# Kernel optimization log

Hardware: AMD Instinct MI355X
Metric: run time of the kernel (lower is better)

The kernel has to match this reference:

```python
import jax, jax.numpy as jnp
import numpy as np

B, N, DIM = 4, 2048, 512
H, DH = 8, 64  # n_heads, dim_head; inner = H*DH = 512
SCALE = DH ** -0.5


def setup_inputs() -> dict:
    key = jax.random.key(0)
    k1, k2, k3 = jax.random.split(key, 3)
    inner = H * DH
    X = jax.random.normal(k1, (B, N, DIM), dtype=jnp.float32)
    W_qkv = jax.random.normal(k2, (DIM, 3 * inner), dtype=jnp.float32) * (DIM ** -0.5)
    W_out = jax.random.normal(k3, (inner, DIM), dtype=jnp.float32) * (inner ** -0.5)
    b_out = jnp.zeros((DIM,), dtype=jnp.float32)
    return {"X": X, "W_qkv": W_qkv, "W_out": W_out, "b_out": b_out}


def reference(X, W_qkv, W_out, b_out):
    # X: (b, n, dim)
    qkv = X @ W_qkv                      # (b, n, 3*h*d)
    q, k, v = jnp.split(qkv, 3, axis=-1)
    def to_heads(t):
        b, n, _ = t.shape
        return t.reshape(b, n, H, DH).transpose(0, 2, 1, 3)  # (b, h, n, d)
    q, k, v = to_heads(q), to_heads(k), to_heads(v)
    # NOTE: original computes scores[n, m] = k_n . q_m and softmaxes over m (query axis)
    scores = jnp.einsum('bhnd,bhmd->bhnm', k, q) * SCALE     # (b, h, n_k, m_q)
    att = jax.nn.softmax(scores, axis=-1)
    # out token axis is the KEY index n: out[n, d] = sum_e att[n, e] * v[e, d]
    out = jnp.einsum('bhne,bhed->bhnd', att, v)              # (b, h, n, d)
    out = out.transpose(0, 2, 1, 3).reshape(X.shape[0], X.shape[1], H * DH)  # (b, n, h*d)
    return out @ W_out + b_out
```

## Files before the change

kernel.cpp:

```cpp
#include <hip/hip_runtime.h>
#include <hip/hip_bf16.h>

typedef __bf16 bf16_t;
typedef bf16_t bf16x8 __attribute__((ext_vector_type(8)));
typedef bf16_t bf16x4v __attribute__((ext_vector_type(4)));
typedef float f32x4 __attribute__((ext_vector_type(4)));
typedef float f32x16 __attribute__((ext_vector_type(16)));
typedef int i32x4 __attribute__((ext_vector_type(4)));

#define B_SZ 4
#define N_TOK 2048
#define DIM 512
#define H_N 8
#define DH 64
#define INNER 512
#define M_ROWS 8192
#define NQKV 1536
#define K_FOLD 0.18033688011112042f

#define GLD_LDS16(gp, lp)                                          \
  __builtin_amdgcn_global_load_lds(                                \
      (const __attribute__((address_space(1))) void*)(gp),         \
      (__attribute__((address_space(3))) void*)(lp), 16, 0, 0)

__device__ __forceinline__ float fexp2(float x) {
#if __has_builtin(__builtin_amdgcn_exp2f)
  return __builtin_amdgcn_exp2f(x);
#else
  float r;
  asm volatile("v_exp_f32 %0, %1\n\ts_nop 1" : "=v"(r) : "v"(x));
  return r;
#endif
}

__device__ __forceinline__ int cvtpk_bf16(float lo, float hi) {
  int r;
  asm("v_cvt_pk_bf16_f32 %0, %1, %2" : "=v"(r) : "v"(lo), "v"(hi));
  return r;
}

__device__ __forceinline__ void permswap32(int& a, int& b) {
  asm volatile("v_permlane32_swap_b32 %0, %1" : "+v"(a), "+v"(b));
}


__global__ void f32_to_bf16_kernel(const float* __restrict__ src,
                                   bf16_t* __restrict__ dst, int n4) {
  int i = blockIdx.x * blockDim.x + threadIdx.x;
  int stride = gridDim.x * blockDim.x;
  for (; i < n4; i += stride) {
    float4 f = reinterpret_cast<const float4*>(src)[i];
    bf16x4v o;
    o.x = (bf16_t)f.x; o.y = (bf16_t)f.y; o.z = (bf16_t)f.z; o.w = (bf16_t)f.w;
    reinterpret_cast<bf16x4v*>(dst)[i] = o;
  }
}

__global__ void transpose_f32_to_bf16_kernel(const float* __restrict__ src,
                                             bf16_t* __restrict__ dst, int R, int C) {
  int t = blockIdx.x * blockDim.x + threadIdx.x;
  if (t >= R * C) return;
  int r = t / C, c = t - r * C;
  dst[(size_t)c * R + r] = (bf16_t)src[t];
}

template <int MODE>
__global__ __launch_bounds__(256) void gemm_bf16_kernel(
    const bf16_t* __restrict__ A, const bf16_t* __restrict__ Bt,
    int M, int Nn, int K,
    bf16_t* __restrict__ qb, bf16_t* __restrict__ kb, bf16_t* __restrict__ vtb,
    float* __restrict__ outF, const float* __restrict__ bias) {
  __shared__ bf16_t As[128 * 64];
  __shared__ bf16_t Bs[128 * 64];

  const int tid = threadIdx.x;
  const int lane = tid & 63;
  const int wave = tid >> 6;
  const int g = lane >> 4, c = lane & 15;
  const int wm = (wave >> 1) * 64, wn = (wave & 1) * 64;
  const int m0 = blockIdx.x * 128, n0 = blockIdx.y * 128;

  f32x4 acc[4][4] = {};

  for (int k0 = 0; k0 < K; k0 += 64) {
    __syncthreads();
    #pragma unroll
    for (int i = 0; i < 4; ++i) {
      int blk = i * 256 + tid;
      int row = blk >> 3;
      int cb = (blk & 7) ^ (row & 7);
      int base = (i * 256 + wave * 64) * 8;
      GLD_LDS16(A + (size_t)(m0 + row) * K + k0 + cb * 8, &As[base]);
      GLD_LDS16(Bt + (size_t)(n0 + row) * K + k0 + cb * 8, &Bs[base]);
    }
    __syncthreads();
    __builtin_amdgcn_s_setprio(1);
    #pragma unroll
    for (int ks = 0; ks < 2; ++ks) {
      bf16x8 af[4], bfr[4];
      #pragma unroll
      for (int i = 0; i < 4; ++i) {
        af[i] = *reinterpret_cast<const bf16x8*>(
            &As[(wm + i * 16 + c) * 64 + (((ks * 4 + g) ^ (c & 7)) * 8)]);
        bfr[i] = *reinterpret_cast<const bf16x8*>(
            &Bs[(wn + i * 16 + c) * 64 + (((ks * 4 + g) ^ (c & 7)) * 8)]);
      }
      #pragma unroll
      for (int mi = 0; mi < 4; ++mi)
        #pragma unroll
        for (int ni = 0; ni < 4; ++ni)
          acc[mi][ni] = __builtin_amdgcn_mfma_f32_16x16x32_bf16(
              af[mi], bfr[ni], acc[mi][ni], 0, 0, 0);
    }
    __builtin_amdgcn_s_setprio(0);
  }

  #pragma unroll
  for (int mi = 0; mi < 4; ++mi) {
    #pragma unroll
    for (int ni = 0; ni < 4; ++ni) {
      int colg = n0 + wn + ni * 16 + c;
      if (MODE == 0) {
        int s = colg >> 9;
        int hh = (colg >> 6) & 7, dd = colg & 63;
        int rowg0 = m0 + wm + mi * 16 + g * 4;
        int bb = rowg0 >> 11, nn = rowg0 & 2047;
        if (s == 2) {
          bf16x4v pk;
          pk.x = (bf16_t)acc[mi][ni][0];
          pk.y = (bf16_t)acc[mi][ni][1];
          pk.z = (bf16_t)acc[mi][ni][2];
          pk.w = (bf16_t)acc[mi][ni][3];
          *reinterpret_cast<bf16x4v*>(
              &vtb[(((size_t)(bb * H_N + hh)) * DH + dd) * N_TOK + nn]) = pk;
        } else {
          float sc = (s == 1) ? K_FOLD : 1.0f;
          bf16_t* dst = (s == 0) ? qb : kb;
          #pragma unroll
          for (int r = 0; r < 4; ++r)
            dst[(((size_t)(bb * H_N + hh)) * N_TOK + nn + r) * DH + dd] =
                (bf16_t)(acc[mi][ni][r] * sc);
        }
      } else {
        #pragma unroll
        for (int r = 0; r < 4; ++r) {
          int rowg = m0 + wm + mi * 16 + g * 4 + r;
          outF[(size_t)rowg * Nn + colg] = acc[mi][ni][r] + bias[colg];
        }
      }
    }
  }
}

__global__ __launch_bounds__(512, 4) void attn_kernel(
    const bf16_t* __restrict__ Qproj, const bf16_t* __restrict__ Kproj,
    const bf16_t* __restrict__ Vt, bf16_t* __restrict__ att_out) {
  const int glin = blockIdx.x;
  const int xcd = glin & 7;
  const int jj = glin >> 3;
  const int hb = xcd * 4 + (jj >> 4);
  const int rb = jj & 15;
  const int h = hb & 7, b = hb >> 3;

  const size_t hbo = (size_t)(b * H_N + h);
  const bf16_t* Aq = Kproj + hbo * N_TOK * DH;
  const bf16_t* Ak = Qproj + hbo * N_TOK * DH;
  const bf16_t* Av = Vt + hbo * (size_t)(DH * N_TOK);

  const int tid = threadIdx.x, lane = tid & 63, wave = tid >> 6;
  const int nl = lane & 31;
  const int hf = lane >> 5;
  const int grp = wave >> 2;
  const int gw = wave & 3;
  const int r0 = rb * 128, wr0 = gw * 32;
  const int kv0 = grp * 1024;

  __shared__ __align__(16) char smem[65536];
  bf16_t* sKg = (bf16_t*)(smem + grp * 32768);
  bf16_t* sVg = (bf16_t*)(smem + grp * 32768 + 16384);

  bf16x8 qreg[4];
  #pragma unroll
  for (int ks = 0; ks < 4; ++ks)
    qreg[ks] = *reinterpret_cast<const bf16x8*>(
        &Aq[(size_t)(r0 + wr0 + nl) * DH + ks * 16 + hf * 8]);

  f32x16 accO0 = {}, accO1 = {};
  float Lp[4] = {};

  const int gtid = tid & 255;
  auto stage = [&](int buf, int j0) {
    #pragma unroll
    for (int i = 0; i < 2; ++i) {
      int idx = i * 256 + gtid;
      int row = idx >> 3;
      int cb = (idx & 7) ^ (row & 7);
      int base = buf * 4096 + (i * 256 + gw * 64) * 8;
      GLD_LDS16(Ak + (size_t)(j0 + row) * DH + cb * 8, sKg + base);
      GLD_LDS16(Av + (size_t)row * N_TOK + j0 + cb * 8, sVg + base);
    }
  };

  stage(0, kv0);
  __syncthreads();

  constexpr int NT = 16;
  for (int t = 0; t < NT; ++t) {
    if (t + 1 < NT) stage((t + 1) & 1, kv0 + (t + 1) * 64);
    const bf16_t* bK = sKg + (t & 1) * 4096;
    const bf16_t* bV = sVg + (t & 1) * 4096;

    f32x16 aT[2] = {};
    __builtin_amdgcn_s_setprio(1);
    #pragma unroll
    for (int ks = 0; ks < 4; ++ks) {
      #pragma unroll
      for (int mi = 0; mi < 2; ++mi) {
        int rowt = mi * 32 + nl;
        bf16x8 ak = *reinterpret_cast<const bf16x8*>(
            &bK[rowt * 64 + (((ks * 2 + hf) ^ (rowt & 7)) * 8)]);
        aT[mi] = __builtin_amdgcn_mfma_f32_32x32x16_bf16(
            ak, qreg[ks], aT[mi], 0, 0, 0);
      }
    }
    __builtin_amdgcn_s_setprio(0);

    #pragma unroll
    for (int r = 0; r < 16; ++r) {
      float p0 = fexp2(aT[0][r]); aT[0][r] = p0;
      float p1 = fexp2(aT[1][r]); aT[1][r] = p1;
      Lp[r & 3] += p0 + p1;
    }

    i32x4 pk[4];
    #pragma unroll
    for (int ks = 0; ks < 4; ++ks) {
      const int mi = ks >> 1, base = (ks & 1) * 8;
      int a0 = cvtpk_bf16(aT[mi][base + 0], aT[mi][base + 1]);
      int b0 = cvtpk_bf16(aT[mi][base + 4], aT[mi][base + 5]);
      int a1 = cvtpk_bf16(aT[mi][base + 2], aT[mi][base + 3]);
      int b1 = cvtpk_bf16(aT[mi][base + 6], aT[mi][base + 7]);
      permswap32(a0, b0);
      permswap32(a1, b1);
      pk[ks].x = a0; pk[ks].y = a1; pk[ks].z = b0; pk[ks].w = b1;
    }

    __builtin_amdgcn_s_setprio(1);
    #pragma unroll
    for (int ks = 0; ks < 4; ++ks) {
      bf16x8 pfrag = __builtin_bit_cast(bf16x8, pk[ks]);
      int rv0 = nl, rv1 = 32 + nl;
      bf16x8 av0 = *reinterpret_cast<const bf16x8*>(
          &bV[rv0 * 64 + (((ks * 2 + hf) ^ (rv0 & 7)) * 8)]);
      bf16x8 av1 = *reinterpret_cast<const bf16x8*>(
          &bV[rv1 * 64 + (((ks * 2 + hf) ^ (rv1 & 7)) * 8)]);
      accO0 = __builtin_amdgcn_mfma_f32_32x32x16_bf16(av0, pfrag, accO0, 0, 0, 0);
      accO1 = __builtin_amdgcn_mfma_f32_32x32x16_bf16(av1, pfrag, accO1, 0, 0, 0);
    }
    __builtin_amdgcn_s_setprio(0);

    __syncthreads();
  }

  float Lsum = (Lp[0] + Lp[1]) + (Lp[2] + Lp[3]);
  float* mb = (float*)smem;
  const int moff = (gw * 64 + lane) * 36;
  if (grp == 1) {
    #pragma unroll
    for (int r = 0; r < 16; ++r) {
      mb[moff + r] = accO0[r];
      mb[moff + 16 + r] = accO1[r];
    }
    mb[moff + 32] = Lsum;
  }
  __syncthreads();
  if (grp == 0) {
    #pragma unroll
    for (int r = 0; r < 16; ++r) {
      accO0[r] += mb[moff + r];
      accO1[r] += mb[moff + 16 + r];
    }
    float l = Lsum + mb[moff + 32];
    l += __shfl_xor(l, 32);
    float invL = 1.0f / l;
    const int nrow = r0 + wr0 + nl;
    #pragma unroll
    for (int q = 0; q < 4; ++q) {
      int d0a = 8 * q + 4 * hf;
      bf16x4v o;
      o.x = (bf16_t)(accO0[4 * q + 0] * invL);
      o.y = (bf16_t)(accO0[4 * q + 1] * invL);
      o.z = (bf16_t)(accO0[4 * q + 2] * invL);
      o.w = (bf16_t)(accO0[4 * q + 3] * invL);
      *reinterpret_cast<bf16x4v*>(
          &att_out[((size_t)(b * N_TOK) + nrow) * INNER + h * DH + d0a]) = o;
      bf16x4v o2;
      o2.x = (bf16_t)(accO1[4 * q + 0] * invL);
      o2.y = (bf16_t)(accO1[4 * q + 1] * invL);
      o2.z = (bf16_t)(accO1[4 * q + 2] * invL);
      o2.w = (bf16_t)(accO1[4 * q + 3] * invL);
      *reinterpret_cast<bf16x4v*>(
          &att_out[((size_t)(b * N_TOK) + nrow) * INNER + h * DH + 32 + d0a]) = o2;
    }
  }
}


extern "C" void kernel_launch(void* const* d_in, const int* in_sizes, int n_in,
                              void* d_out, int out_size, void* d_ws, size_t ws_size,
                              hipStream_t stream) {
  const float* X    = (const float*)d_in[0];
  const float* Wqkv = (const float*)d_in[1];
  const float* Wout = (const float*)d_in[2];
  const float* bout = (const float*)d_in[3];
  float* out = (float*)d_out;

  char* ws = (char*)d_ws;
  bf16_t* Xb    = (bf16_t*)(ws);
  bf16_t* WqkvT = (bf16_t*)(ws + 8388608);
  bf16_t* WoutT = (bf16_t*)(ws + 9961472);
  bf16_t* Qb    = (bf16_t*)(ws + 10485760);
  bf16_t* Kb    = (bf16_t*)(ws + 18874368);
  bf16_t* Vtb   = (bf16_t*)(ws + 27262976);
  bf16_t* AttO  = (bf16_t*)(ws + 35651584);

  f32_to_bf16_kernel<<<2048, 256, 0, stream>>>(X, Xb, (M_ROWS * DIM) / 4);
  transpose_f32_to_bf16_kernel<<<(DIM * NQKV + 255) / 256, 256, 0, stream>>>(
      Wqkv, WqkvT, DIM, NQKV);
  transpose_f32_to_bf16_kernel<<<(INNER * DIM + 255) / 256, 256, 0, stream>>>(
      Wout, WoutT, INNER, DIM);

  dim3 g1(M_ROWS / 128, NQKV / 128);
  gemm_bf16_kernel<0><<<g1, 256, 0, stream>>>(Xb, WqkvT, M_ROWS, NQKV, DIM,
                                              Qb, Kb, Vtb, nullptr, nullptr);

  attn_kernel<<<dim3(512), 512, 0, stream>>>(Qb, Kb, Vtb, AttO);

  dim3 g3(M_ROWS / 128, DIM / 128);
  gemm_bf16_kernel<1><<<g3, 256, 0, stream>>>(AttO, WoutT, M_ROWS, DIM, DIM,
                                              nullptr, nullptr, nullptr, out, bout);
}
```

Measured before the change: 90.46 us.

## Split GEMM into QKV and 64-row output kernels, prefetch V fragments in attention

The templated GEMM is split into a dedicated QKV-projection kernel and a new output-projection kernel with 64-row tiles. The smaller tiles double the block count for the 8192x512 output GEMM so more CUs are busy. In the attention loop, V fragments are loaded from LDS before the QK MFMAs, and the P conversion is interleaved directly with the PV MFMAs, hiding LDS latency at the cost of extra registers. The merge buffer stride changes from 36 to 37 floats to reduce LDS bank conflicts.

```diff
diff --git a/kernel.cpp b/kernel.cpp
--- a/kernel.cpp
+++ b/kernel.cpp
@@ -64,12 +64,9 @@
   dst[(size_t)c * R + r] = (bf16_t)src[t];
 }
 
-template <int MODE>
-__global__ __launch_bounds__(256) void gemm_bf16_kernel(
-    const bf16_t* __restrict__ A, const bf16_t* __restrict__ Bt,
-    int M, int Nn, int K,
-    bf16_t* __restrict__ qb, bf16_t* __restrict__ kb, bf16_t* __restrict__ vtb,
-    float* __restrict__ outF, const float* __restrict__ bias) {
+__global__ __launch_bounds__(256) void gemm_qkv_kernel(
+    const bf16_t* __restrict__ A, const bf16_t* __restrict__ Bt, int K,
+    bf16_t* __restrict__ qb, bf16_t* __restrict__ kb, bf16_t* __restrict__ vtb) {
   __shared__ bf16_t As[128 * 64];
   __shared__ bf16_t Bs[128 * 64];
 
@@ -120,33 +117,95 @@
     #pragma unroll
     for (int ni = 0; ni < 4; ++ni) {
       int colg = n0 + wn + ni * 16 + c;
-      if (MODE == 0) {
-        int s = colg >> 9;
-        int hh = (colg >> 6) & 7, dd = colg & 63;
-        int rowg0 = m0 + wm + mi * 16 + g * 4;
-        int bb = rowg0 >> 11, nn = rowg0 & 2047;
-        if (s == 2) {
-          bf16x4v pk;
-          pk.x = (bf16_t)acc[mi][ni][0];
-          pk.y = (bf16_t)acc[mi][ni][1];
-          pk.z = (bf16_t)acc[mi][ni][2];
-          pk.w = (bf16_t)acc[mi][ni][3];
-          *reinterpret_cast<bf16x4v*>(
-              &vtb[(((size_t)(bb * H_N + hh)) * DH + dd) * N_TOK + nn]) = pk;
-        } else {
-          float sc = (s == 1) ? K_FOLD : 1.0f;
-          bf16_t* dst = (s == 0) ? qb : kb;
-          #pragma unroll
-          for (int r = 0; r < 4; ++r)
-            dst[(((size_t)(bb * H_N + hh)) * N_TOK + nn + r) * DH + dd] =
-                (bf16_t)(acc[mi][ni][r] * sc);
-        }
+      int s = colg >> 9;
+      int hh = (colg >> 6) & 7, dd = colg & 63;
+      int rowg0 = m0 + wm + mi * 16 + g * 4;
+      int bb = rowg0 >> 11, nn = rowg0 & 2047;
+      if (s == 2) {
+        bf16x4v pk;
+        pk.x = (bf16_t)acc[mi][ni][0];
+        pk.y = (bf16_t)acc[mi][ni][1];
+        pk.z = (bf16_t)acc[mi][ni][2];
+        pk.w = (bf16_t)acc[mi][ni][3];
+        *reinterpret_cast<bf16x4v*>(
+            &vtb[(((size_t)(bb * H_N + hh)) * DH + dd) * N_TOK + nn]) = pk;
       } else {
+        float sc = (s == 1) ? K_FOLD : 1.0f;
+        bf16_t* dst = (s == 0) ? qb : kb;
         #pragma unroll
-        for (int r = 0; r < 4; ++r) {
-          int rowg = m0 + wm + mi * 16 + g * 4 + r;
-          outF[(size_t)rowg * Nn + colg] = acc[mi][ni][r] + bias[colg];
-        }
+        for (int r = 0; r < 4; ++r)
+          dst[(((size_t)(bb * H_N + hh)) * N_TOK + nn + r) * DH + dd] =
+              (bf16_t)(acc[mi][ni][r] * sc);
+      }
+    }
+  }
+}
+
+__global__ __launch_bounds__(256) void gemm_out_kernel(
+    const bf16_t* __restrict__ A, const bf16_t* __restrict__ Bt,
+    float* __restrict__ outF, const float* __restrict__ bias) {
+  __shared__ bf16_t As[64 * 64];
+  __shared__ bf16_t Bs[128 * 64];
+
+  const int tid = threadIdx.x;
+  const int lane = tid & 63;
+  const int wave = tid >> 6;
+  const int g = lane >> 4, c = lane & 15;
+  const int wm = (wave >> 1) * 32, wn = (wave & 1) * 64;
+  const int m0 = blockIdx.x * 64, n0 = blockIdx.y * 128;
+
+  f32x4 acc[2][4] = {};
+
+  for (int k0 = 0; k0 < DIM; k0 += 64) {
+    __syncthreads();
+    #pragma unroll
+    for (int i = 0; i < 2; ++i) {
+      int blk = i * 256 + tid;
+      int row = blk >> 3;
+      int cb = (blk & 7) ^ (row & 7);
+      int base = (i * 256 + wave * 64) * 8;
+      GLD_LDS16(A + (size_t)(m0 + row) * DIM + k0 + cb * 8, &As[base]);
+    }
+    #pragma unroll
+    for (int i = 0; i < 4; ++i) {
+      int blk = i * 256 + tid;
+      int row = blk >> 3;
+      int cb = (blk & 7) ^ (row & 7);
+      int base = (i * 256 + wave * 64) * 8;
+      GLD_LDS16(Bt + (size_t)(n0 + row) * DIM + k0 + cb * 8, &Bs[base]);
+    }
+    __syncthreads();
+    __builtin_amdgcn_s_setprio(1);
+    #pragma unroll
+    for (int ks = 0; ks < 2; ++ks) {
+      bf16x8 af[2], bfr[4];
+      #pragma unroll
+      for (int i = 0; i < 2; ++i)
+        af[i] = *reinterpret_cast<const bf16x8*>(
+            &As[(wm + i * 16 + c) * 64 + (((ks * 4 + g) ^ (c & 7)) * 8)]);
+      #pragma unroll
+      for (int i = 0; i < 4; ++i)
+        bfr[i] = *reinterpret_cast<const bf16x8*>(
+            &Bs[(wn + i * 16 + c) * 64 + (((ks * 4 + g) ^ (c & 7)) * 8)]);
+      #pragma unroll
+      for (int mi = 0; mi < 2; ++mi)
+        #pragma unroll
+        for (int ni = 0; ni < 4; ++ni)
+          acc[mi][ni] = __builtin_amdgcn_mfma_f32_16x16x32_bf16(
+              af[mi], bfr[ni], acc[mi][ni], 0, 0, 0);
+    }
+    __builtin_amdgcn_s_setprio(0);
+  }
+
+  #pragma unroll
+  for (int mi = 0; mi < 2; ++mi) {
+    #pragma unroll
+    for (int ni = 0; ni < 4; ++ni) {
+      int colg = n0 + wn + ni * 16 + c;
+      #pragma unroll
+      for (int r = 0; r < 4; ++r) {
+        int rowg = m0 + wm + mi * 16 + g * 4 + r;
+        outF[(size_t)rowg * DIM + colg] = acc[mi][ni][r] + bias[colg];
       }
     }
   }
@@ -210,6 +269,15 @@
     const bf16_t* bK = sKg + (t & 1) * 4096;
     const bf16_t* bV = sVg + (t & 1) * 4096;
 
+    bf16x8 av[2][4];
+    #pragma unroll
+    for (int ks = 0; ks < 4; ++ks) {
+      av[0][ks] = *reinterpret_cast<const bf16x8*>(
+          &bV[nl * 64 + (((ks * 2 + hf) ^ (nl & 7)) * 8)]);
+      av[1][ks] = *reinterpret_cast<const bf16x8*>(
+          &bV[(32 + nl) * 64 + (((ks * 2 + hf) ^ (nl & 7)) * 8)]);
+    }
+
     f32x16 aT[2] = {};
     __builtin_amdgcn_s_setprio(1);
     #pragma unroll
@@ -232,7 +300,7 @@
       Lp[r & 3] += p0 + p1;
     }
 
-    i32x4 pk[4];
+    __builtin_amdgcn_s_setprio(1);
     #pragma unroll
     for (int ks = 0; ks < 4; ++ks) {
       const int mi = ks >> 1, base = (ks & 1) * 8;
@@ -242,20 +310,10 @@
       int b1 = cvtpk_bf16(aT[mi][base + 6], aT[mi][base + 7]);
       permswap32(a0, b0);
       permswap32(a1, b1);
-      pk[ks].x = a0; pk[ks].y = a1; pk[ks].z = b0; pk[ks].w = b1;
-    }
-
-    __builtin_amdgcn_s_setprio(1);
-    #pragma unroll
-    for (int ks = 0; ks < 4; ++ks) {
-      bf16x8 pfrag = __builtin_bit_cast(bf16x8, pk[ks]);
-      int rv0 = nl, rv1 = 32 + nl;
-      bf16x8 av0 = *reinterpret_cast<const bf16x8*>(
-          &bV[rv0 * 64 + (((ks * 2 + hf) ^ (rv0 & 7)) * 8)]);
-      bf16x8 av1 = *reinterpret_cast<const bf16x8*>(
-          &bV[rv1 * 64 + (((ks * 2 + hf) ^ (rv1 & 7)) * 8)]);
-      accO0 = __builtin_amdgcn_mfma_f32_32x32x16_bf16(av0, pfrag, accO0, 0, 0, 0);
-      accO1 = __builtin_amdgcn_mfma_f32_32x32x16_bf16(av1, pfrag, accO1, 0, 0, 0);
+      i32x4 w; w.x = a0; w.y = a1; w.z = b0; w.w = b1;
+      bf16x8 pfrag = __builtin_bit_cast(bf16x8, w);
+      accO0 = __builtin_amdgcn_mfma_f32_32x32x16_bf16(av[0][ks], pfrag, accO0, 0, 0, 0);
+      accO1 = __builtin_amdgcn_mfma_f32_32x32x16_bf16(av[1][ks], pfrag, accO1, 0, 0, 0);
     }
     __builtin_amdgcn_s_setprio(0);
 
@@ -264,7 +322,7 @@
 
   float Lsum = (Lp[0] + Lp[1]) + (Lp[2] + Lp[3]);
   float* mb = (float*)smem;
-  const int moff = (gw * 64 + lane) * 36;
+  const int moff = (gw * 64 + lane) * 37;
   if (grp == 1) {
     #pragma unroll
     for (int r = 0; r < 16; ++r) {
@@ -331,12 +389,10 @@
       Wout, WoutT, INNER, DIM);
 
   dim3 g1(M_ROWS / 128, NQKV / 128);
-  gemm_bf16_kernel<0><<<g1, 256, 0, stream>>>(Xb, WqkvT, M_ROWS, NQKV, DIM,
-                                              Qb, Kb, Vtb, nullptr, nullptr);
+  gemm_qkv_kernel<<<g1, 256, 0, stream>>>(Xb, WqkvT, DIM, Qb, Kb, Vtb);
 
   attn_kernel<<<dim3(512), 512, 0, stream>>>(Qb, Kb, Vtb, AttO);
 
-  dim3 g3(M_ROWS / 128, DIM / 128);
-  gemm_bf16_kernel<1><<<g3, 256, 0, stream>>>(AttO, WoutT, M_ROWS, DIM, DIM,
-                                              nullptr, nullptr, nullptr, out, bout);
-}
+  dim3 g3(M_ROWS / 64, DIM / 128);
+  gemm_out_kernel<<<g3, 256, 0, stream>>>(AttO, WoutT, out, bout);
+}
```

After: 100.8 us. +11.4%, slower.
